# Performance work log

Measured on AMD Instinct MI355X. Metric: run time of the kernel, lower is better.

## Reference

```python
import jax, jax.numpy as jnp
import numpy as np

CHANNELS = 32
CONVOLUTIONS = 8
GIN_HIDDEN = 64
HIDDEN = 64
NODE_TYPES = 6
OUTPUT = 32
N_NODES = 200000
N_EDGES = 3200000
NUM_GRAPHS = 512
EPS = 1e-5


def setup_inputs() -> dict:
    key = jax.random.key(0)
    ks = jax.random.split(key, 16)
    x = jax.random.randint(ks[0], (N_NODES,), 0, NODE_TYPES)
    edge_index = jax.random.randint(ks[1], (2, N_EDGES), 0, N_NODES)
    batch = jnp.sort(jax.random.randint(ks[2], (N_NODES,), 0, NUM_GRAPHS))
    s = lambda fan_in: 1.0 / np.sqrt(fan_in)
    emb = jax.random.normal(ks[3], (NODE_TYPES, CHANNELS), jnp.float32)
    Wh = jax.random.uniform(ks[4], (CONVOLUTIONS, CHANNELS, GIN_HIDDEN), jnp.float32, -s(CHANNELS), s(CHANNELS))
    bh = jax.random.uniform(ks[5], (CONVOLUTIONS, GIN_HIDDEN), jnp.float32, -s(CHANNELS), s(CHANNELS))
    Wo = jax.random.uniform(ks[6], (CONVOLUTIONS, GIN_HIDDEN, CHANNELS), jnp.float32, -s(GIN_HIDDEN), s(GIN_HIDDEN))
    bo = jax.random.uniform(ks[7], (CONVOLUTIONS, CHANNELS), jnp.float32, -s(GIN_HIDDEN), s(GIN_HIDDEN))
    fin = (CONVOLUTIONS + 1) * CHANNELS
    W_hid = jax.random.uniform(ks[8], (fin, HIDDEN), jnp.float32, -s(fin), s(fin))
    b_hid = jax.random.uniform(ks[9], (HIDDEN,), jnp.float32, -s(fin), s(fin))
    W_out = jax.random.uniform(ks[10], (HIDDEN, OUTPUT), jnp.float32, -s(HIDDEN), s(HIDDEN))
    b_out = jax.random.uniform(ks[11], (OUTPUT,), jnp.float32, -s(HIDDEN), s(HIDDEN))
    return {"x": x, "edge_index": edge_index, "batch": batch, "emb": emb,
            "Wh": Wh, "bh": bh, "Wo": Wo, "bo": bo,
            "W_hid": W_hid, "b_hid": b_hid, "W_out": W_out, "b_out": b_out}


def reference(x, edge_index, batch, emb, Wh, bh, Wo, bo, W_hid, b_hid, W_out, b_out):
    n = x.shape[0]
    src, dst = edge_index[0], edge_index[1]
    counts = jax.ops.segment_sum(jnp.ones((n,), jnp.float32), batch,
                                 num_segments=NUM_GRAPHS)[:, None]  # [G,1]
    h = emb[x]  # [N, C]
    xs = [h]
    for i in range(CONVOLUTIONS):
        # GINConv (eps=0): MLP(x + sum_{j->i} x_j)
        aggr = jax.ops.segment_sum(h[src], dst, num_segments=n)
        z = h + aggr
        z = jax.nn.relu(z @ Wh[i] + bh[i]) @ Wo[i] + bo[i]
        # per-graph InstanceNorm (no affine, biased variance)
        mean = jax.ops.segment_sum(z, batch, num_segments=NUM_GRAPHS) / counts
        var = jax.ops.segment_sum(z * z, batch, num_segments=NUM_GRAPHS) / counts - mean * mean
        zn = (z - mean[batch]) * jax.lax.rsqrt(var[batch] + EPS)
        h = jax.nn.relu(h + zn)
        xs.append(h)
    feats = jnp.concatenate(xs, axis=1)  # [N, (CONVOLUTIONS+1)*C]
    pooled = jax.ops.segment_max(feats, batch, num_segments=NUM_GRAPHS)  # [G, 288]
    hid = jax.nn.relu(pooled @ W_hid + b_hid)
    return hid @ W_out + b_out  # [G, OUTPUT]
```

## Files before the change

### kernel.cpp

```cpp
#include <hip/hip_runtime.h>
#include <math.h>

#define NGRAPH 512
#define FEATS 288
#define EPS 1e-5f
#define NBAND 4
#define MAXBUCK 32
#define BREP 4
#define BSHIFT 13
#define SUBR 1024
#define IMGCAP 20480

typedef __attribute__((ext_vector_type(8))) short short8v;
typedef __attribute__((ext_vector_type(8))) unsigned short ushort8v;
typedef __attribute__((ext_vector_type(4))) unsigned short ushort4v;
typedef __attribute__((ext_vector_type(4))) float float4v;

__device__ __forceinline__ unsigned short f2bf(float f) {
  unsigned int u = __float_as_uint(f);
  u += 0x7fff + ((u >> 16) & 1);
  return (unsigned short)(u >> 16);
}
__device__ __forceinline__ float bf2f(unsigned short u) {
  return __uint_as_float(((unsigned int)u) << 16);
}

__device__ __forceinline__ int srcband(int s, int bandsz) {
  return (s >= bandsz) + (s >= 2 * bandsz) + (s >= 3 * bandsz);
}

__device__ __forceinline__ void atomicMaxF(float* addr, float v) {
  if (v >= 0.f) atomicMax((int*)addr, __float_as_int(v));
  else atomicMin((unsigned int*)addr, __float_as_uint(v));
}

__global__ void k_init(float* __restrict__ pooled, float* __restrict__ counts,
                       float* __restrict__ stats, int* __restrict__ degseg,
                       int* __restrict__ typemask, unsigned int* __restrict__ curpk,
                       int* __restrict__ bucketcnt,
                       const float* __restrict__ Wh, const float* __restrict__ Wo,
                       unsigned short* __restrict__ whb, unsigned short* __restrict__ wob,
                       int N4, int N) {
  int i = blockIdx.x * blockDim.x + threadIdx.x;
  if (i < NGRAPH * FEATS) pooled[i] = -INFINITY;
  if (i < NGRAPH) { counts[i] = 0.f; typemask[i] = 0; }
  if (i < NGRAPH * 128) stats[i] = 0.f;
  if (i < N4) degseg[i] = 0;
  if (i < N) curpk[i] = 0u;
  if (i < BREP * MAXBUCK) bucketcnt[i] = 0;

  if (blockIdx.x < 8) {
    int conv = blockIdx.x;
    const float* wh = Wh + (size_t)conv * 2048;
    const float* wo = Wo + (size_t)conv * 2048;
    unsigned short* oh = whb + (size_t)conv * 2048;
    unsigned short* oo = wob + (size_t)conv * 2048;
    for (int p = threadIdx.x; p < 2048; p += blockDim.x) {
      int rem = p & 511, l = rem >> 3, ii = rem & 7;
      int nt = p >> 9;
      int k = (l >> 4) * 8 + ii;
      int n = nt * 16 + (l & 15);
      oh[p] = f2bf(wh[k * 64 + n]);
      int blk = p >> 9, nt2 = blk >> 1, ks = blk & 1;
      int k2 = ks * 32 + (l >> 4) * 8 + ii;
      int n2 = nt2 * 16 + (l & 15);
      oo[p] = f2bf(wo[k2 * 32 + n2]);
    }
  }
}

__global__ __launch_bounds__(256) void k_embed(
    const int* __restrict__ x, const int* __restrict__ batch,
    const float* __restrict__ emb, unsigned short* __restrict__ hbf,
    int* __restrict__ typemask, float* __restrict__ counts, int N) {
  long t = (long)blockIdx.x * blockDim.x + threadIdx.x;
  int n = (int)(t >> 3), q = (int)(t & 7);
  int lane = threadIdx.x & 63;
  bool valid = (n < N);
  int g = 0, tt = 0;
  if (valid) {
    g = batch[n];
    tt = x[n];
    float4 e = *((const float4*)(emb + (size_t)tt * 32 + q * 4));
    ushort4v hb;
    hb[0] = f2bf(e.x); hb[1] = f2bf(e.y); hb[2] = f2bf(e.z); hb[3] = f2bf(e.w);
    *((ushort4v*)(hbf + (size_t)n * 32 + q * 4)) = hb;
  }
  int g0 = __shfl(g, 0);
  bool uniform = __all(valid) && __all(g == g0);
  int m = valid ? (1 << tt) : 0;
  if (uniform) {
    #pragma unroll
    for (int d = 1; d < 64; d <<= 1) m |= __shfl_xor(m, d);
    if (lane == 0) {
      atomicOr(&typemask[g0], m);
      atomicAdd(&counts[g0], 8.f);
    }
  } else if (valid && q == 0) {
    atomicOr(&typemask[g], m);
    atomicAdd(&counts[g], 1.f);
  }
}

__global__ void k_pool0(const int* __restrict__ typemask, const float* __restrict__ emb,
                        float* __restrict__ pooled) {
  int i = blockIdx.x * blockDim.x + threadIdx.x;
  if (i >= NGRAPH * 32) return;
  int g = i >> 5, c = i & 31;
  int m = typemask[g];
  float v = -INFINITY;
  #pragma unroll
  for (int t = 0; t < 6; t++)
    if (m & (1 << t)) v = fmaxf(v, emb[t * 32 + c]);
  pooled[(size_t)g * FEATS + c] = v;
}

__global__ __launch_bounds__(256) void k_bin(
    const int* __restrict__ src, const int* __restrict__ dst, int E,
    int cap4, int* __restrict__ bucketcnt, unsigned int* __restrict__ ebuf,
    int bandsz) {
  __shared__ int lcnt[MAXBUCK];
  __shared__ int gbase[MAXBUCK];
  for (int i = threadIdx.x; i < MAXBUCK; i += 256) lcnt[i] = 0;
  __syncthreads();
  int e0 = blockIdx.x * 2048 + threadIdx.x;
  int bArr[8], rArr[8];
  unsigned int pArr[8];
  #pragma unroll
  for (int it = 0; it < 8; it++) {
    int e = e0 + it * 256;
    bArr[it] = -1;
    if (e < E) {
      int d = dst[e];
      int s = src[e];
      int b = d >> BSHIFT;
      int sb = srcband(s, bandsz);
      pArr[it] = ((unsigned int)(d & ((1 << BSHIFT) - 1)) << 18)
               | ((unsigned int)sb << 16) | (unsigned int)(s - sb * bandsz);
      rArr[it] = atomicAdd(&lcnt[b], 1);
      bArr[it] = b;
    }
  }
  __syncthreads();
  int rep = blockIdx.x & (BREP - 1);
  if (threadIdx.x < MAXBUCK) {
    int b = threadIdx.x;
    int c = lcnt[b];
    gbase[b] = (c > 0) ? atomicAdd(&bucketcnt[rep * MAXBUCK + b], c) : 0;
  }
  __syncthreads();
  #pragma unroll
  for (int it = 0; it < 8; it++) {
    if (bArr[it] >= 0) {
      int b = bArr[it];
      int pos = gbase[b] + rArr[it];
      if (pos < cap4)
        ebuf[((size_t)b * BREP + rep) * cap4 + pos] = pArr[it];
    }
  }
}

__global__ __launch_bounds__(1024) void k_histL(
    const unsigned int* __restrict__ ebuf, const int* __restrict__ bucketcnt,
    int cap4, int* __restrict__ degseg, int N) {
  __shared__ unsigned int cpk[SUBR];
  int p = blockIdx.x >> 3;
  int j = blockIdx.x & 7;
  int node0 = (p << BSHIFT) + j * SUBR;
  if (node0 >= N) return;
  int nEnd = min(node0 + SUBR, N);
  for (int i = threadIdx.x; i < SUBR; i += 1024) cpk[i] = 0u;
  __syncthreads();
  for (int rep = 0; rep < BREP; rep++) {
    int c = min(bucketcnt[rep * MAXBUCK + p], cap4);
    const unsigned int* base = ebuf + ((size_t)p * BREP + rep) * cap4;
    for (int idx = threadIdx.x; idx < c; idx += 1024) {
      unsigned int pk = base[idx];
      int node = (p << BSHIFT) + (int)(pk >> 18);
      if (node >= node0 && node < nEnd) {
        int sb = (int)((pk >> 16) & 3u);
        atomicAdd(&cpk[node - node0], 1u << (sb * 8));
      }
    }
  }
  __syncthreads();
  for (int i = threadIdx.x; i < nEnd - node0; i += 1024) {
    unsigned int v = cpk[i];
    int* dp = degseg + (size_t)(node0 + i) * 4;
    dp[0] = (int)(v & 0xffu);
    dp[1] = (int)((v >> 8) & 0xffu);
    dp[2] = (int)((v >> 16) & 0xffu);
    dp[3] = (int)(v >> 24);
  }
}

__global__ __launch_bounds__(1024) void k_scatL(
    const unsigned int* __restrict__ ebuf, const int* __restrict__ bucketcnt,
    int cap4, const int* __restrict__ rowseg, unsigned int* __restrict__ curpk,
    unsigned short* __restrict__ adj, int E, int N) {
  __shared__ unsigned short img[IMGCAP];
  __shared__ unsigned int cpk[SUBR];
  int p = blockIdx.x >> 3;
  int j = blockIdx.x & 7;
  int node0 = (p << BSHIFT) + j * SUBR;
  if (node0 >= N) return;
  int nEnd = min(node0 + SUBR, N);
  int imgbase = rowseg[(size_t)node0 * 4];
  int imgend = (nEnd < N) ? rowseg[(size_t)nEnd * 4] : E;
  int isz = imgend - imgbase;
  bool lds = (isz <= IMGCAP);
  for (int i = threadIdx.x; i < SUBR; i += 1024) cpk[i] = 0u;
  __syncthreads();
  for (int rep = 0; rep < BREP; rep++) {
    int c = min(bucketcnt[rep * MAXBUCK + p], cap4);
    const unsigned int* base = ebuf + ((size_t)p * BREP + rep) * cap4;
    for (int idx = threadIdx.x; idx < c; idx += 1024) {
      unsigned int pk = base[idx];
      int node = (p << BSHIFT) + (int)(pk >> 18);
      if (node >= node0 && node < nEnd) {
        int sb = (int)((pk >> 16) & 3u);
        int seg = node * 4 + sb;
        unsigned short srel = (unsigned short)(pk & 0xffffu);
        if (lds) {
          unsigned int old = atomicAdd(&cpk[node - node0], 1u << (sb * 8));
          int rank = (int)((old >> (sb * 8)) & 0xffu);
          img[rowseg[seg] + rank - imgbase] = srel;
        } else {
          unsigned int old = atomicAdd(&curpk[seg >> 2], 1u << ((seg & 3) * 8));
          int rank = (int)((old >> ((seg & 3) * 8)) & 0xffu);
          adj[rowseg[seg] + rank] = srel;
        }
      }
    }
  }
  __syncthreads();
  if (lds) {
    for (int i = threadIdx.x; i < isz; i += 1024)
      adj[imgbase + i] = img[i];
  }
}

__global__ void k_hist(const int* __restrict__ dst, const int* __restrict__ src,
                       int* __restrict__ degseg, int E, int eb,
                       int dband, int bandsz, int N) {
  int band = blockIdx.x / eb;
  int e = (blockIdx.x - band * eb) * blockDim.x + threadIdx.x;
  if (e >= E) return;
  int bandlo = band * dband;
  int bandhi = min(bandlo + dband, N);
  int d = dst[e];
  if (d < bandlo || d >= bandhi) return;
  int sb = srcband(src[e], bandsz);
  atomicAdd(&degseg[(size_t)d * 4 + sb], 1);
}

__global__ void k_scatter(const int* __restrict__ src, const int* __restrict__ dst,
                          const int* __restrict__ rowseg, unsigned int* __restrict__ curpk,
                          unsigned short* __restrict__ adj, int E,
                          int eb, int dband, int bandsz, int N) {
  int band = blockIdx.x / eb;
  int e = (blockIdx.x - band * eb) * blockDim.x + threadIdx.x;
  if (e >= E) return;
  int bandlo = band * dband;
  int bandhi = min(bandlo + dband, N);
  int d = dst[e];
  if (d < bandlo || d >= bandhi) return;
  int s = src[e];
  int sb = srcband(s, bandsz);
  int seg = d * 4 + sb;
  unsigned int old = atomicAdd(&curpk[seg >> 2], 1u << ((seg & 3) * 8));
  int local = (int)((old >> ((seg & 3) * 8)) & 0xffu);
  adj[rowseg[seg] + local] = (unsigned short)(s - sb * bandsz);
}

__global__ void k_scan_block(const int* __restrict__ deg, int* __restrict__ excl,
                             int* __restrict__ bsum, int N) {
  __shared__ int s[256];
  int i = blockIdx.x * 256 + threadIdx.x;
  int t = threadIdx.x;
  int v = (i < N) ? deg[i] : 0;
  s[t] = v;
  __syncthreads();
  for (int off = 1; off < 256; off <<= 1) {
    int add = (t >= off) ? s[t - off] : 0;
    __syncthreads();
    s[t] += add;
    __syncthreads();
  }
  if (i < N) excl[i] = s[t] - v;
  if (t == 255) bsum[blockIdx.x] = s[255];
}

__global__ void k_scan_bsum(int* __restrict__ bsum, int nb) {
  __shared__ int s[256];
  __shared__ int carry;
  int t = threadIdx.x;
  if (t == 0) carry = 0;
  __syncthreads();
  for (int base = 0; base < nb; base += 256) {
    int i = base + t;
    int v = (i < nb) ? bsum[i] : 0;
    s[t] = v;
    __syncthreads();
    for (int off = 1; off < 256; off <<= 1) {
      int add = (t >= off) ? s[t - off] : 0;
      __syncthreads();
      s[t] += add;
      __syncthreads();
    }
    if (i < nb) bsum[i] = s[t] - v + carry;
    __syncthreads();
    if (t == 0) carry += s[255];
    __syncthreads();
  }
}

__global__ void k_scan_add(int* __restrict__ excl, const int* __restrict__ bsum, int N) {
  int i = blockIdx.x * 256 + threadIdx.x;
  if (i < N) excl[i] = excl[i] + bsum[blockIdx.x];
}

__global__ __launch_bounds__(256, 8) void k_conv(
    const unsigned short* __restrict__ hbf,
    const unsigned short* __restrict__ adj, const int* __restrict__ rowseg,
    const int* __restrict__ degseg,
    const unsigned short* __restrict__ whb, const float* __restrict__ bh,
    const unsigned short* __restrict__ wob, const float* __restrict__ bo,
    const int* __restrict__ batch, unsigned short* __restrict__ z2,
    float* __restrict__ stats, float* __restrict__ statsOther,
    int bandsz, int N) {
  __shared__ unsigned short sWhB[4 * 64 * 8];
  __shared__ unsigned short sWoB[2 * 2 * 64 * 8];
  __shared__ unsigned short st[4][16][72];

  {
    int zi = blockIdx.x * 256 + threadIdx.x;
    if (zi < NGRAPH * 64) statsOther[zi] = 0.f;
    int p = threadIdx.x * 8;
    *((ushort8v*)&sWhB[p]) = *((const ushort8v*)&whb[p]);
    *((ushort8v*)&sWoB[p]) = *((const ushort8v*)&wob[p]);
  }
  __syncthreads();

  int wid = threadIdx.x >> 6;
  int lane = threadIdx.x & 63;
  int col = lane & 15;
  int grp = lane >> 4;
  int gwave = blockIdx.x * 4 + wid;
  int wstride = gridDim.x * 4;
  int ntiles = (N + 15) >> 4;

  const unsigned short* __restrict__ qb = hbf + grp * 8;

  float keepT[2][8];
  #pragma unroll
  for (int t = 0; t < 2; t++)
    #pragma unroll
    for (int i = 0; i < 8; i++) keepT[t][i] = 0.f;

  #pragma unroll
  for (int b = 0; b < 4; b++) {
    const unsigned short* __restrict__ bq = qb + (size_t)(b * bandsz) * 32;
    #pragma unroll
    for (int t = 0; t < 2; t++) {
      int tile = gwave + t * wstride;
      if (tile >= ntiles) continue;
      int node = tile * 16 + col;
      int s0 = 0, dg = 0;
      if (node < N) {
        s0 = rowseg[(size_t)node * 4 + b];
        dg = degseg[(size_t)node * 4 + b];
      }
      int k = 0;
      for (; k + 4 <= dg; k += 4) {
        int sA = adj[s0 + k + 0];
        int sB = adj[s0 + k + 1];
        int sC = adj[s0 + k + 2];
        int sD = adj[s0 + k + 3];
        ushort8v a = *((const ushort8v*)(bq + (size_t)sA * 32));
        ushort8v bv = *((const ushort8v*)(bq + (size_t)sB * 32));
        ushort8v c = *((const ushort8v*)(bq + (size_t)sC * 32));
        ushort8v d = *((const ushort8v*)(bq + (size_t)sD * 32));
        #pragma unroll
        for (int i = 0; i < 8; i++) {
          keepT[t][i] += bf2f(a[i]);
          keepT[t][i] += bf2f(bv[i]);
          keepT[t][i] += bf2f(c[i]);
          keepT[t][i] += bf2f(d[i]);
        }
      }
      if (k + 2 <= dg) {
        int sA = adj[s0 + k + 0];
        int sB = adj[s0 + k + 1];
        ushort8v a = *((const ushort8v*)(bq + (size_t)sA * 32));
        ushort8v bv = *((const ushort8v*)(bq + (size_t)sB * 32));
        #pragma unroll
        for (int i = 0; i < 8; i++) {
          keepT[t][i] += bf2f(a[i]);
          keepT[t][i] += bf2f(bv[i]);
        }
        k += 2;
      }
      if (k < dg) {
        int sA = adj[s0 + k];
        ushort8v a = *((const ushort8v*)(bq + (size_t)sA * 32));
        #pragma unroll
        for (int i = 0; i < 8; i++) keepT[t][i] += bf2f(a[i]);
      }
    }
  }

  #pragma unroll
  for (int t = 0; t < 2; t++) {
    int tile = gwave + t * wstride;
    if (tile >= ntiles) continue;
    int base = tile * 16;
    int node = base + col;

    float zf[8];
    if (node < N) {
      ushort8v own = *((const ushort8v*)(hbf + (size_t)node * 32 + grp * 8));
      #pragma unroll
      for (int i = 0; i < 8; i++) zf[i] = bf2f(own[i]) + keepT[t][i];
    } else {
      #pragma unroll
      for (int i = 0; i < 8; i++) zf[i] = 0.f;
    }
    short8v afrag;
    #pragma unroll
    for (int i = 0; i < 8; i++) afrag[i] = (short)f2bf(zf[i]);

    #pragma unroll
    for (int nt = 0; nt < 4; nt++) {
      float b = bh[nt * 16 + col];
      float4v acc1 = {b, b, b, b};
      short8v bfrag = *((const short8v*)&sWhB[(nt * 64 + lane) * 8]);
      acc1 = __builtin_amdgcn_mfma_f32_16x16x32_bf16(afrag, bfrag, acc1, 0, 0, 0);
      #pragma unroll
      for (int r = 0; r < 4; r++) {
        st[wid][grp * 4 + r][nt * 16 + col] = f2bf(fmaxf(acc1[r], 0.f));
      }
    }

    short8v a2[2];
    #pragma unroll
    for (int ks = 0; ks < 2; ks++)
      a2[ks] = *((const short8v*)&st[wid][col][ks * 32 + grp * 8]);

    float4v acc2[2];
    #pragma unroll
    for (int nt2 = 0; nt2 < 2; nt2++) {
      float b = bo[nt2 * 16 + col];
      acc2[nt2] = (float4v){b, b, b, b};
      #pragma unroll
      for (int ks = 0; ks < 2; ks++) {
        short8v bfrag = *((const short8v*)&sWoB[((nt2 * 2 + ks) * 64 + lane) * 8]);
        acc2[nt2] = __builtin_amdgcn_mfma_f32_16x16x32_bf16(a2[ks], bfrag, acc2[nt2], 0, 0, 0);
      }
    }

    #pragma unroll
    for (int nt2 = 0; nt2 < 2; nt2++) {
      #pragma unroll
      for (int r = 0; r < 4; r++) {
        int nd = base + grp * 4 + r;
        if (nd < N)
          __builtin_nontemporal_store(f2bf(acc2[nt2][r]), z2 + (size_t)nd * 32 + nt2 * 16 + col);
      }
    }

    int g0 = batch[base];
    int gLast = batch[min(base + 15, N - 1)];
    if ((base + 16 <= N) && g0 == gLast) {
      #pragma unroll
      for (int nt2 = 0; nt2 < 2; nt2++) {
        float s = acc2[nt2][0] + acc2[nt2][1] + acc2[nt2][2] + acc2[nt2][3];
        float ss = acc2[nt2][0] * acc2[nt2][0] + acc2[nt2][1] * acc2[nt2][1]
                 + acc2[nt2][2] * acc2[nt2][2] + acc2[nt2][3] * acc2[nt2][3];
        s += __shfl_xor(s, 16); s += __shfl_xor(s, 32);
        ss += __shfl_xor(ss, 16); ss += __shfl_xor(ss, 32);
        if (grp == 0) {
          atomicAdd(&stats[(size_t)g0 * 64 + nt2 * 16 + col], s);
          atomicAdd(&stats[(size_t)g0 * 64 + 32 + nt2 * 16 + col], ss);
        }
      }
    } else {
      #pragma unroll
      for (int nt2 = 0; nt2 < 2; nt2++) {
        #pragma unroll
        for (int r = 0; r < 4; r++) {
          int nd = base + grp * 4 + r;
          if (nd < N) {
            int g = batch[nd];
            float v = acc2[nt2][r];
            atomicAdd(&stats[(size_t)g * 64 + nt2 * 16 + col], v);
            atomicAdd(&stats[(size_t)g * 64 + 32 + nt2 * 16 + col], v * v);
          }
        }
      }
    }
  }
}

__global__ __launch_bounds__(256, 4) void k_conv0(
    const unsigned short* __restrict__ hbf,
    const unsigned short* __restrict__ adj, const int* __restrict__ rowseg,
    const int* __restrict__ degseg,
    const int* __restrict__ x, const float* __restrict__ emb,
    const unsigned short* __restrict__ whb, const float* __restrict__ bh,
    const unsigned short* __restrict__ wob, const float* __restrict__ bo,
    const int* __restrict__ batch, unsigned short* __restrict__ z2,
    float* __restrict__ stats, float* __restrict__ statsOther,
    int bandsz, int N) {
  __shared__ unsigned short sWhB[4 * 64 * 8];
  __shared__ unsigned short sWoB[2 * 2 * 64 * 8];
  __shared__ unsigned short st[4][16][72];
  __shared__ float sEmb[6][32];

  {
    int zi = blockIdx.x * 256 + threadIdx.x;
    if (zi < NGRAPH * 64) statsOther[zi] = 0.f;
    int p = threadIdx.x * 8;
    *((ushort8v*)&sWhB[p]) = *((const ushort8v*)&whb[p]);
    *((ushort8v*)&sWoB[p]) = *((const ushort8v*)&wob[p]);
    if (threadIdx.x < 192) ((float*)sEmb)[threadIdx.x] = emb[threadIdx.x];
  }
  __syncthreads();

  int wid = threadIdx.x >> 6;
  int lane = threadIdx.x & 63;
  int tile = blockIdx.x * 4 + wid;
  int base = tile * 16;
  if (base >= N) return;
  int col = lane & 15;
  int grp = lane >> 4;
  int node = base + col;

  int sArr[4] = {0, 0, 0, 0}, dArr[4] = {0, 0, 0, 0};
  if (node < N) {
    int4 s4 = *((const int4*)(rowseg + (size_t)node * 4));
    int4 d4 = *((const int4*)(degseg + (size_t)node * 4));
    sArr[0] = s4.x; sArr[1] = s4.y; sArr[2] = s4.z; sArr[3] = s4.w;
    dArr[0] = d4.x; dArr[1] = d4.y; dArr[2] = d4.z; dArr[3] = d4.w;
  }

  float c0 = 0.f, c1 = 0.f, c2 = 0.f, c3 = 0.f, c4 = 0.f, c5 = 0.f;
  #pragma unroll
  for (int b = 0; b < 4; b++) {
    int s0 = sArr[b], dg = dArr[b];
    int bbase = b * bandsz;
    for (int j = grp; j < dg; j += 4) {
      int sA = bbase + (int)adj[s0 + j];
      int tA = x[sA];
      c0 += (tA == 0) ? 1.f : 0.f; c1 += (tA == 1) ? 1.f : 0.f;
      c2 += (tA == 2) ? 1.f : 0.f; c3 += (tA == 3) ? 1.f : 0.f;
      c4 += (tA == 4) ? 1.f : 0.f; c5 += (tA == 5) ? 1.f : 0.f;
    }
  }

  c0 += __shfl_xor(c0, 16); c0 += __shfl_xor(c0, 32);
  c1 += __shfl_xor(c1, 16); c1 += __shfl_xor(c1, 32);
  c2 += __shfl_xor(c2, 16); c2 += __shfl_xor(c2, 32);
  c3 += __shfl_xor(c3, 16); c3 += __shfl_xor(c3, 32);
  c4 += __shfl_xor(c4, 16); c4 += __shfl_xor(c4, 32);
  c5 += __shfl_xor(c5, 16); c5 += __shfl_xor(c5, 32);

  float zf[8];
  if (node < N) {
    ushort8v own = *((const ushort8v*)(hbf + (size_t)node * 32 + grp * 8));
    #pragma unroll
    for (int i = 0; i < 8; i++) {
      int ch = grp * 8 + i;
      float v = bf2f(own[i]);
      v = fmaf(c0, sEmb[0][ch], v);
      v = fmaf(c1, sEmb[1][ch], v);
      v = fmaf(c2, sEmb[2][ch], v);
      v = fmaf(c3, sEmb[3][ch], v);
      v = fmaf(c4, sEmb[4][ch], v);
      v = fmaf(c5, sEmb[5][ch], v);
      zf[i] = v;
    }
  } else {
    #pragma unroll
    for (int i = 0; i < 8; i++) zf[i] = 0.f;
  }
  short8v afrag;
  #pragma unroll
  for (int i = 0; i < 8; i++) afrag[i] = (short)f2bf(zf[i]);

  #pragma unroll
  for (int nt = 0; nt < 4; nt++) {
    float b = bh[nt * 16 + col];
    float4v acc1 = {b, b, b, b};
    short8v bfrag = *((const short8v*)&sWhB[(nt * 64 + lane) * 8]);
    acc1 = __builtin_amdgcn_mfma_f32_16x16x32_bf16(afrag, bfrag, acc1, 0, 0, 0);
    #pragma unroll
    for (int r = 0; r < 4; r++) {
      st[wid][grp * 4 + r][nt * 16 + col] = f2bf(fmaxf(acc1[r], 0.f));
    }
  }

  short8v a2[2];
  #pragma unroll
  for (int ks = 0; ks < 2; ks++)
    a2[ks] = *((const short8v*)&st[wid][col][ks * 32 + grp * 8]);

  float4v acc2[2];
  #pragma unroll
  for (int nt2 = 0; nt2 < 2; nt2++) {
    float b = bo[nt2 * 16 + col];
    acc2[nt2] = (float4v){b, b, b, b};
    #pragma unroll
    for (int ks = 0; ks < 2; ks++) {
      short8v bfrag = *((const short8v*)&sWoB[((nt2 * 2 + ks) * 64 + lane) * 8]);
      acc2[nt2] = __builtin_amdgcn_mfma_f32_16x16x32_bf16(a2[ks], bfrag, acc2[nt2], 0, 0, 0);
    }
  }

  #pragma unroll
  for (int nt2 = 0; nt2 < 2; nt2++) {
    #pragma unroll
    for (int r = 0; r < 4; r++) {
      int nd = base + grp * 4 + r;
      if (nd < N)
        __builtin_nontemporal_store(f2bf(acc2[nt2][r]), z2 + (size_t)nd * 32 + nt2 * 16 + col);
    }
  }

  int g0 = batch[base];
  int gLast = batch[min(base + 15, N - 1)];
  if ((base + 16 <= N) && g0 == gLast) {
    #pragma unroll
    for (int nt2 = 0; nt2 < 2; nt2++) {
      float s = acc2[nt2][0] + acc2[nt2][1] + acc2[nt2][2] + acc2[nt2][3];
      float ss = acc2[nt2][0] * acc2[nt2][0] + acc2[nt2][1] * acc2[nt2][1]
               + acc2[nt2][2] * acc2[nt2][2] + acc2[nt2][3] * acc2[nt2][3];
      s += __shfl_xor(s, 16); s += __shfl_xor(s, 32);
      ss += __shfl_xor(ss, 16); ss += __shfl_xor(ss, 32);
      if (grp == 0) {
        atomicAdd(&stats[(size_t)g0 * 64 + nt2 * 16 + col], s);
        atomicAdd(&stats[(size_t)g0 * 64 + 32 + nt2 * 16 + col], ss);
      }
    }
  } else {
    #pragma unroll
    for (int nt2 = 0; nt2 < 2; nt2++) {
      #pragma unroll
      for (int r = 0; r < 4; r++) {
        int nd = base + grp * 4 + r;
        if (nd < N) {
          int g = batch[nd];
          float v = acc2[nt2][r];
          atomicAdd(&stats[(size_t)g * 64 + nt2 * 16 + col], v);
          atomicAdd(&stats[(size_t)g * 64 + 32 + nt2 * 16 + col], v * v);
        }
      }
    }
  }
}

__global__ __launch_bounds__(256) void k_norm(
    unsigned short* __restrict__ hbf, const unsigned short* __restrict__ z2,
    const float* __restrict__ stats, const float* __restrict__ counts,
    const int* __restrict__ batch, float* __restrict__ pooled, int conv, int N) {
  long t = (long)blockIdx.x * blockDim.x + threadIdx.x;
  int n = (int)(t >> 3), q = (int)(t & 7);
  int lane = threadIdx.x & 63;
  bool valid = (n < N);

  int g = 0;
  float r0 = -INFINITY, r1 = -INFINITY, r2 = -INFINITY, r3 = -INFINITY;
  if (valid) {
    g = batch[n];
    float cnt = counts[g];
    float4 sv = *((const float4*)(stats + (size_t)g * 64 + q * 4));
    float4 qv = *((const float4*)(stats + (size_t)g * 64 + 32 + q * 4));
    float m0 = 0.f, m1 = 0.f, m2 = 0.f, m3 = 0.f;
    float i0 = 0.f, i1 = 0.f, i2 = 0.f, i3 = 0.f;
    if (cnt > 0.f) {
      m0 = sv.x / cnt; m1 = sv.y / cnt; m2 = sv.z / cnt; m3 = sv.w / cnt;
      i0 = rsqrtf(fmaxf(qv.x / cnt - m0 * m0, 0.f) + EPS);
      i1 = rsqrtf(fmaxf(qv.y / cnt - m1 * m1, 0.f) + EPS);
      i2 = rsqrtf(fmaxf(qv.z / cnt - m2 * m2, 0.f) + EPS);
      i3 = rsqrtf(fmaxf(qv.w / cnt - m3 * m3, 0.f) + EPS);
    }
    ushort4v hb = *((const ushort4v*)(hbf + (size_t)n * 32 + q * 4));
    ushort4v zv = *((const ushort4v*)(z2 + (size_t)n * 32 + q * 4));
    r0 = fmaxf(bf2f(hb[0]) + (bf2f(zv[0]) - m0) * i0, 0.f);
    r1 = fmaxf(bf2f(hb[1]) + (bf2f(zv[1]) - m1) * i1, 0.f);
    r2 = fmaxf(bf2f(hb[2]) + (bf2f(zv[2]) - m2) * i2, 0.f);
    r3 = fmaxf(bf2f(hb[3]) + (bf2f(zv[3]) - m3) * i3, 0.f);
    hb[0] = f2bf(r0); hb[1] = f2bf(r1); hb[2] = f2bf(r2); hb[3] = f2bf(r3);
    *((ushort4v*)(hbf + (size_t)n * 32 + q * 4)) = hb;
  }

  int g0 = __shfl(g, 0);
  bool uniform = __all(valid) && __all(g == g0);
  if (uniform) {
    float m0 = r0, m1 = r1, m2 = r2, m3 = r3;
    #pragma unroll
    for (int d = 8; d < 64; d <<= 1) {
      m0 = fmaxf(m0, __shfl_xor(m0, d));
      m1 = fmaxf(m1, __shfl_xor(m1, d));
      m2 = fmaxf(m2, __shfl_xor(m2, d));
      m3 = fmaxf(m3, __shfl_xor(m3, d));
    }
    if (lane < 8) {
      float* poolrow = pooled + (size_t)g0 * FEATS + (conv + 1) * 32 + lane * 4;
      atomicMaxF(poolrow + 0, m0);
      atomicMaxF(poolrow + 1, m1);
      atomicMaxF(poolrow + 2, m2);
      atomicMaxF(poolrow + 3, m3);
    }
  } else if (valid) {
    float* poolrow = pooled + (size_t)g * FEATS + (conv + 1) * 32 + q * 4;
    atomicMaxF(poolrow + 0, r0);
    atomicMaxF(poolrow + 1, r1);
    atomicMaxF(poolrow + 2, r2);
    atomicMaxF(poolrow + 3, r3);
  }
}

__global__ __launch_bounds__(64) void k_head(
    const float* __restrict__ pooled, const float* __restrict__ W_hid,
    const float* __restrict__ b_hid, const float* __restrict__ W_out,
    const float* __restrict__ b_out, float* __restrict__ out) {
  __shared__ float sp[FEATS];
  __shared__ float sh[64];
  int g = blockIdx.x;
  for (int i = threadIdx.x; i < FEATS; i += 64) sp[i] = pooled[(size_t)g * FEATS + i];
  __syncthreads();
  int j = threadIdx.x;
  float acc = b_hid[j];
  for (int k = 0; k < FEATS; k++) acc = fmaf(sp[k], W_hid[k * 64 + j], acc);
  sh[j] = fmaxf(acc, 0.f);
  __syncthreads();
  if (j < 32) {
    float o = b_out[j];
    #pragma unroll
    for (int k = 0; k < 64; k++) o = fmaf(sh[k], W_out[k * 32 + j], o);
    out[(size_t)g * 32 + j] = o;
  }
}

extern "C" void kernel_launch(void* const* d_in, const int* in_sizes, int n_in,
                              void* d_out, int out_size, void* d_ws, size_t ws_size,
                              hipStream_t stream) {
  const int* x      = (const int*)d_in[0];
  const int* edge   = (const int*)d_in[1];
  const int* batch  = (const int*)d_in[2];
  const float* emb  = (const float*)d_in[3];
  const float* Wh   = (const float*)d_in[4];
  const float* bh   = (const float*)d_in[5];
  const float* Wo   = (const float*)d_in[6];
  const float* bo   = (const float*)d_in[7];
  const float* W_hid = (const float*)d_in[8];
  const float* b_hid = (const float*)d_in[9];
  const float* W_out = (const float*)d_in[10];
  const float* b_out = (const float*)d_in[11];
  float* out = (float*)d_out;

  int N = in_sizes[0];
  int E = in_sizes[1] / 2;
  const int* src = edge;
  const int* dst = edge + E;

  int N4 = N * 4;
  int bandsz = (N + NBAND - 1) / NBAND;
  int nbuck = (N + (1 << BSHIFT) - 1) >> BSHIFT;
  int cap4 = E / (nbuck * BREP) + 8000;

  float* ws = (float*)d_ws;
  size_t off = 0;
  unsigned short* z2 = (unsigned short*)(ws + off); off += (size_t)N * 16;
  float* pooled  = ws + off; off += (size_t)NGRAPH * FEATS;
  float* stats   = ws + off; off += (size_t)NGRAPH * 128;
  float* counts  = ws + off; off += NGRAPH;
  unsigned short* hbf = (unsigned short*)(ws + off); off += (size_t)N * 16;
  unsigned short* whb = (unsigned short*)(ws + off); off += 8192;
  unsigned short* wob = (unsigned short*)(ws + off); off += 8192;
  int* iws = (int*)(ws + off);
  size_t ioff = 0;
  int* degseg   = iws + ioff; ioff += N4;
  int* rowseg   = iws + ioff; ioff += N4;
  unsigned int* curpk = (unsigned int*)(iws + ioff); ioff += N;
  unsigned short* adj = (unsigned short*)(iws + ioff); ioff += (E + 1) / 2;
  int* bsum     = iws + ioff; ioff += 4096;
  int* typemask = iws + ioff; ioff += NGRAPH;
  int* bucketcnt = iws + ioff; ioff += BREP * MAXBUCK;
  unsigned int* ebuf = (unsigned int*)(iws + ioff); ioff += (size_t)nbuck * BREP * cap4;
  bool fastCSR = ((off + ioff) * sizeof(float) <= ws_size) && (nbuck <= MAXBUCK)
               && (bandsz < 65536);

  int eb = (E + 255) / 256;
  int eb8 = (E + 2047) / 2048;
  int nb4 = (N4 + 255) / 256;
  int nb8 = (int)(((size_t)N * 8 + 255) / 256);
  int tiles = (N + 15) / 16;
  int mb = (tiles + 3) / 4;
  int ib = nb4;
  if (ib < (NGRAPH * FEATS + 255) / 256) ib = (NGRAPH * FEATS + 255) / 256;

  int dband = (N + NBAND - 1) / NBAND;

  k_init<<<ib, 256, 0, stream>>>(pooled, counts, stats, degseg, typemask, curpk,
                                 bucketcnt, Wh, Wo, whb, wob, N4, N);
  k_embed<<<nb8, 256, 0, stream>>>(x, batch, emb, hbf, typemask, counts, N);
  k_pool0<<<(NGRAPH * 32 + 255) / 256, 256, 0, stream>>>(typemask, emb, pooled);

  if (fastCSR) {
    k_bin<<<eb8, 256, 0, stream>>>(src, dst, E, cap4, bucketcnt, ebuf, bandsz);
    k_histL<<<nbuck * 8, 1024, 0, stream>>>(ebuf, bucketcnt, cap4, degseg, N);
    k_scan_block<<<nb4, 256, 0, stream>>>(degseg, rowseg, bsum, N4);
    k_scan_bsum<<<1, 256, 0, stream>>>(bsum, nb4);
    k_scan_add<<<nb4, 256, 0, stream>>>(rowseg, bsum, N4);
    k_scatL<<<nbuck * 8, 1024, 0, stream>>>(ebuf, bucketcnt, cap4, rowseg, curpk,
                                            adj, E, N);
  } else {
    k_hist<<<NBAND * eb, 256, 0, stream>>>(dst, src, degseg, E, eb, dband, bandsz, N);
    k_scan_block<<<nb4, 256, 0, stream>>>(degseg, rowseg, bsum, N4);
    k_scan_bsum<<<1, 256, 0, stream>>>(bsum, nb4);
    k_scan_add<<<nb4, 256, 0, stream>>>(rowseg, bsum, N4);
    k_scatter<<<NBAND * eb, 256, 0, stream>>>(src, dst, rowseg, curpk, adj, E, eb,
                                              dband, bandsz, N);
  }

  const int GCONV = 2048;

  for (int i = 0; i < 8; i++) {
    float* sCur = stats + (size_t)(i & 1) * NGRAPH * 64;
    float* sOth = stats + (size_t)((i + 1) & 1) * NGRAPH * 64;
    if (i == 0) {
      k_conv0<<<mb, 256, 0, stream>>>(hbf, adj, rowseg, degseg, x, emb,
                                      whb, bh, wob, bo,
                                      batch, z2, sCur, sOth, bandsz, N);
    } else {
      k_conv<<<GCONV, 256, 0, stream>>>(hbf, adj, rowseg, degseg,
                                        whb + (size_t)i * 2048, bh + (size_t)i * 64,
                                        wob + (size_t)i * 2048, bo + (size_t)i * 32,
                                        batch, z2, sCur, sOth, bandsz, N);
    }
    k_norm<<<nb8, 256, 0, stream>>>(hbf, z2, sCur, counts, batch, pooled, i, N);
  }
  k_head<<<NGRAPH, 64, 0, stream>>>(pooled, W_hid, b_hid, W_out, b_out, out);
}
```

Measured before the change: 841.1 us.

## Add second binning pass so CSR hist/scatter blocks read only their sub-range

```diff
diff --git a/kernel.cpp b/kernel.cpp
--- a/kernel.cpp
+++ b/kernel.cpp
@@ -37,10 +37,10 @@
 __global__ void k_init(float* __restrict__ pooled, float* __restrict__ counts,
                        float* __restrict__ stats, int* __restrict__ degseg,
                        int* __restrict__ typemask, unsigned int* __restrict__ curpk,
-                       int* __restrict__ bucketcnt,
+                       int* __restrict__ bucketcnt, int* __restrict__ subcnt,
                        const float* __restrict__ Wh, const float* __restrict__ Wo,
                        unsigned short* __restrict__ whb, unsigned short* __restrict__ wob,
-                       int N4, int N) {
+                       int N4, int N, int nsub) {
   int i = blockIdx.x * blockDim.x + threadIdx.x;
   if (i < NGRAPH * FEATS) pooled[i] = -INFINITY;
   if (i < NGRAPH) { counts[i] = 0.f; typemask[i] = 0; }
@@ -48,6 +48,7 @@
   if (i < N4) degseg[i] = 0;
   if (i < N) curpk[i] = 0u;
   if (i < BREP * MAXBUCK) bucketcnt[i] = 0;
+  if (i < nsub) subcnt[i] = 0;
 
   if (blockIdx.x < 8) {
     int conv = blockIdx.x;
@@ -160,28 +161,59 @@
   }
 }
 
-__global__ __launch_bounds__(1024) void k_histL(
+__global__ __launch_bounds__(1024) void k_bin2(
     const unsigned int* __restrict__ ebuf, const int* __restrict__ bucketcnt,
-    int cap4, int* __restrict__ degseg, int N) {
+    int cap4, int* __restrict__ subcnt, unsigned int* __restrict__ ebuf2,
+    int cap2) {
+  __shared__ int lcnt[8];
+  __shared__ int gbase[8];
+  int p = blockIdx.x >> 2;
+  int rep = blockIdx.x & 3;
+  int cnt = min(bucketcnt[rep * MAXBUCK + p], cap4);
+  const unsigned int* base = ebuf + ((size_t)p * BREP + rep) * cap4;
+  for (int c0 = 0; c0 < cnt; c0 += 1024) {
+    if (threadIdx.x < 8) lcnt[threadIdx.x] = 0;
+    __syncthreads();
+    int idx = c0 + threadIdx.x;
+    int j = -1, rank = 0;
+    unsigned int pk = 0;
+    if (idx < cnt) {
+      pk = base[idx];
+      j = (int)((pk >> 28) & 7u);
+      rank = atomicAdd(&lcnt[j], 1);
+    }
+    __syncthreads();
+    if (threadIdx.x < 8) {
+      int c = lcnt[threadIdx.x];
+      gbase[threadIdx.x] = (c > 0) ? atomicAdd(&subcnt[p * 8 + threadIdx.x], c) : 0;
+    }
+    __syncthreads();
+    if (j >= 0) {
+      int pos = gbase[j] + rank;
+      if (pos < cap2)
+        ebuf2[(size_t)(p * 8 + j) * cap2 + pos] = pk;
+    }
+    __syncthreads();
+  }
+}
+
+__global__ __launch_bounds__(1024) void k_histL2(
+    const unsigned int* __restrict__ ebuf2, const int* __restrict__ subcnt,
+    int cap2, int* __restrict__ degseg, int N) {
   __shared__ unsigned int cpk[SUBR];
-  int p = blockIdx.x >> 3;
-  int j = blockIdx.x & 7;
-  int node0 = (p << BSHIFT) + j * SUBR;
+  int s = blockIdx.x;
+  int node0 = s << 10;
   if (node0 >= N) return;
   int nEnd = min(node0 + SUBR, N);
   for (int i = threadIdx.x; i < SUBR; i += 1024) cpk[i] = 0u;
   __syncthreads();
-  for (int rep = 0; rep < BREP; rep++) {
-    int c = min(bucketcnt[rep * MAXBUCK + p], cap4);
-    const unsigned int* base = ebuf + ((size_t)p * BREP + rep) * cap4;
-    for (int idx = threadIdx.x; idx < c; idx += 1024) {
-      unsigned int pk = base[idx];
-      int node = (p << BSHIFT) + (int)(pk >> 18);
-      if (node >= node0 && node < nEnd) {
-        int sb = (int)((pk >> 16) & 3u);
-        atomicAdd(&cpk[node - node0], 1u << (sb * 8));
-      }
-    }
+  int cnt = min(subcnt[s], cap2);
+  const unsigned int* base = ebuf2 + (size_t)s * cap2;
+  for (int idx = threadIdx.x; idx < cnt; idx += 1024) {
+    unsigned int pk = base[idx];
+    int local = (int)((pk >> 18) & 1023u);
+    int sb = (int)((pk >> 16) & 3u);
+    atomicAdd(&cpk[local], 1u << (sb * 8));
   }
   __syncthreads();
   for (int i = threadIdx.x; i < nEnd - node0; i += 1024) {
@@ -194,15 +226,14 @@
   }
 }
 
-__global__ __launch_bounds__(1024) void k_scatL(
-    const unsigned int* __restrict__ ebuf, const int* __restrict__ bucketcnt,
-    int cap4, const int* __restrict__ rowseg, unsigned int* __restrict__ curpk,
+__global__ __launch_bounds__(1024) void k_scatL2(
+    const unsigned int* __restrict__ ebuf2, const int* __restrict__ subcnt,
+    int cap2, const int* __restrict__ rowseg, unsigned int* __restrict__ curpk,
     unsigned short* __restrict__ adj, int E, int N) {
   __shared__ unsigned short img[IMGCAP];
   __shared__ unsigned int cpk[SUBR];
-  int p = blockIdx.x >> 3;
-  int j = blockIdx.x & 7;
-  int node0 = (p << BSHIFT) + j * SUBR;
+  int s = blockIdx.x;
+  int node0 = s << 10;
   if (node0 >= N) return;
   int nEnd = min(node0 + SUBR, N);
   int imgbase = rowseg[(size_t)node0 * 4];
@@ -211,26 +242,23 @@
   bool lds = (isz <= IMGCAP);
   for (int i = threadIdx.x; i < SUBR; i += 1024) cpk[i] = 0u;
   __syncthreads();
-  for (int rep = 0; rep < BREP; rep++) {
-    int c = min(bucketcnt[rep * MAXBUCK + p], cap4);
-    const unsigned int* base = ebuf + ((size_t)p * BREP + rep) * cap4;
-    for (int idx = threadIdx.x; idx < c; idx += 1024) {
-      unsigned int pk = base[idx];
-      int node = (p << BSHIFT) + (int)(pk >> 18);
-      if (node >= node0 && node < nEnd) {
-        int sb = (int)((pk >> 16) & 3u);
-        int seg = node * 4 + sb;
-        unsigned short srel = (unsigned short)(pk & 0xffffu);
-        if (lds) {
-          unsigned int old = atomicAdd(&cpk[node - node0], 1u << (sb * 8));
-          int rank = (int)((old >> (sb * 8)) & 0xffu);
-          img[rowseg[seg] + rank - imgbase] = srel;
-        } else {
-          unsigned int old = atomicAdd(&curpk[seg >> 2], 1u << ((seg & 3) * 8));
-          int rank = (int)((old >> ((seg & 3) * 8)) & 0xffu);
-          adj[rowseg[seg] + rank] = srel;
-        }
-      }
+  int cnt = min(subcnt[s], cap2);
+  const unsigned int* base = ebuf2 + (size_t)s * cap2;
+  for (int idx = threadIdx.x; idx < cnt; idx += 1024) {
+    unsigned int pk = base[idx];
+    int local = (int)((pk >> 18) & 1023u);
+    int sb = (int)((pk >> 16) & 3u);
+    int node = node0 + local;
+    int seg = node * 4 + sb;
+    unsigned short srel = (unsigned short)(pk & 0xffffu);
+    if (lds) {
+      unsigned int old = atomicAdd(&cpk[local], 1u << (sb * 8));
+      int rank = (int)((old >> (sb * 8)) & 0xffu);
+      img[rowseg[seg] + rank - imgbase] = srel;
+    } else {
+      unsigned int old = atomicAdd(&curpk[seg >> 2], 1u << ((seg & 3) * 8));
+      int rank = (int)((old >> ((seg & 3) * 8)) & 0xffu);
+      adj[rowseg[seg] + rank] = srel;
     }
   }
   __syncthreads();
@@ -768,7 +796,9 @@
   int N4 = N * 4;
   int bandsz = (N + NBAND - 1) / NBAND;
   int nbuck = (N + (1 << BSHIFT) - 1) >> BSHIFT;
+  int nsub = nbuck * 8;
   int cap4 = E / (nbuck * BREP) + 8000;
+  int cap2 = E / nsub + 2048;
 
   float* ws = (float*)d_ws;
   size_t off = 0;
@@ -788,7 +818,9 @@
   int* bsum     = iws + ioff; ioff += 4096;
   int* typemask = iws + ioff; ioff += NGRAPH;
   int* bucketcnt = iws + ioff; ioff += BREP * MAXBUCK;
+  int* subcnt   = iws + ioff; ioff += nsub;
   unsigned int* ebuf = (unsigned int*)(iws + ioff); ioff += (size_t)nbuck * BREP * cap4;
+  unsigned int* ebuf2 = (unsigned int*)(iws + ioff); ioff += (size_t)nsub * cap2;
   bool fastCSR = ((off + ioff) * sizeof(float) <= ws_size) && (nbuck <= MAXBUCK)
                && (bandsz < 65536);
 
@@ -804,18 +836,18 @@
   int dband = (N + NBAND - 1) / NBAND;
 
   k_init<<<ib, 256, 0, stream>>>(pooled, counts, stats, degseg, typemask, curpk,
-                                 bucketcnt, Wh, Wo, whb, wob, N4, N);
+                                 bucketcnt, subcnt, Wh, Wo, whb, wob, N4, N, nsub);
   k_embed<<<nb8, 256, 0, stream>>>(x, batch, emb, hbf, typemask, counts, N);
   k_pool0<<<(NGRAPH * 32 + 255) / 256, 256, 0, stream>>>(typemask, emb, pooled);
 
   if (fastCSR) {
     k_bin<<<eb8, 256, 0, stream>>>(src, dst, E, cap4, bucketcnt, ebuf, bandsz);
-    k_histL<<<nbuck * 8, 1024, 0, stream>>>(ebuf, bucketcnt, cap4, degseg, N);
+    k_bin2<<<nbuck * BREP, 1024, 0, stream>>>(ebuf, bucketcnt, cap4, subcnt, ebuf2, cap2);
+    k_histL2<<<nsub, 1024, 0, stream>>>(ebuf2, subcnt, cap2, degseg, N);
     k_scan_block<<<nb4, 256, 0, stream>>>(degseg, rowseg, bsum, N4);
     k_scan_bsum<<<1, 256, 0, stream>>>(bsum, nb4);
     k_scan_add<<<nb4, 256, 0, stream>>>(rowseg, bsum, N4);
-    k_scatL<<<nbuck * 8, 1024, 0, stream>>>(ebuf, bucketcnt, cap4, rowseg, curpk,
-                                            adj, E, N);
+    k_scatL2<<<nsub, 1024, 0, stream>>>(ebuf2, subcnt, cap2, rowseg, curpk, adj, E, N);
   } else {
     k_hist<<<NBAND * eb, 256, 0, stream>>>(dst, src, degseg, E, eb, dband, bandsz, N);
     k_scan_block<<<nb4, 256, 0, stream>>>(degseg, rowseg, bsum, N4);
```

After: 765.8 us, median of 2. 1.1x faster.
